# Performance work log

Measured on AMD Instinct MI355X. Metric: run time of the kernel, lower is better.

The kernel has to match this reference:

```python
import jax, jax.numpy as jnp
import numpy as np

B, S, DIM = 1, 4096, 4096
H, HL, D = 32, 8, 128          # query heads, kv heads (GQA), head_dim
BS = 8                          # sparse_block_size
SINK_TOK, WIN_TOK = 30, 30
HEAVY = 800                     # heavy_const -> Mb = HEAVY // BS top blocks
NEG = -1e30


def setup_inputs() -> dict:
    key = jax.random.key(0)
    k0, k1, k2, k3 = jax.random.split(key, 4)
    x = jax.random.normal(k0, (B, S, DIM), jnp.float32)
    freqs_cis = jax.random.uniform(k1, (S, D // 2, 2), jnp.float32)  # (cos,sin)-like pairs
    wqkv_w = jax.random.normal(k2, ((H + 2 * HL) * D, DIM), jnp.float32) * 0.02
    wo_w = jax.random.normal(k3, (DIM, DIM), jnp.float32) * 0.02
    input_pos = jnp.arange(S, dtype=jnp.int32)
    return {"x": x, "freqs_cis": freqs_cis, "wqkv_w": wqkv_w, "wo_w": wo_w, "input_pos": input_pos}


def _rope(x, fc):
    # x: [B,S,h,D], fc: [S,D/2,2]
    xr = x.reshape(*x.shape[:-1], -1, 2)            # [B,S,h,D/2,2]
    fc = fc[None, :, None]                           # [1,S,1,D/2,2]
    out = jnp.stack([xr[..., 0] * fc[..., 0] - xr[..., 1] * fc[..., 1],
                     xr[..., 1] * fc[..., 0] + xr[..., 0] * fc[..., 1]], axis=-1)
    return out.reshape(x.shape)


def reference(x, freqs_cis, wqkv_w, wo_w, input_pos):
    rep = H // HL
    Tb = (S + BS - 1) // BS
    scale = 1.0 / jnp.sqrt(jnp.float32(D))

    qkv = x @ wqkv_w.T                               # [B,S,(H+2HL)*D]
    q, k, v = jnp.split(qkv, [H * D, (H + HL) * D], axis=-1)
    q = q.reshape(B, S, H, D)
    k = k.reshape(B, S, HL, D)
    v = v.reshape(B, S, HL, D)
    q = _rope(q, freqs_cis)
    k = _rope(k, freqs_cis)

    # ---- block accumulators (KVCache.update_tokens), vectorized ----
    blk = input_pos // BS                            # [S]
    k_sum = jax.ops.segment_sum(jnp.swapaxes(k, 0, 1), blk, num_segments=Tb)  # [Tb,B,HL,D]
    cnt = jax.ops.segment_sum(jnp.ones((S,), jnp.float32), blk, num_segments=Tb)  # [Tb]
    k_rep = k_sum / jnp.maximum(cnt, 1.0)[:, None, None, None]                # block-mean keys
    k_rep_h = jnp.repeat(k_rep, rep, axis=2)        # [Tb,B,H,D] (GQA repeat)

    # ---- per-(B,H) block routing scores ----
    q_mean = q.mean(axis=1)                          # [B,H,D]
    scores = jnp.einsum('bhd,tbhd->bht', q_mean, k_rep_h) * scale  # [B,H,Tb]
    scores = jnp.where(cnt[None, None, :] > 0, scores, NEG)

    # ---- build_block_index: sink + window + topk ----
    sink_b = min((min(SINK_TOK, S) + BS - 1) // BS, Tb)
    window_b = min((min(WIN_TOK, S) + BS - 1) // BS, Tb)
    cur_block = (S - 1) // BS
    win_start = max(0, cur_block - window_b + 1)
    win_end = cur_block + 1
    sink_ids = jnp.arange(sink_b, dtype=jnp.int32)
    window_ids = jnp.arange(win_start, win_end, dtype=jnp.int32)
    Mb = max(0, min(HEAVY // BS, Tb))
    sc = scores.at[..., :sink_b].set(NEG).at[..., window_ids].set(NEG)
    top_ids = jax.lax.top_k(sc, Mb)[1].astype(jnp.int32)                      # [B,H,Mb]
    bidx = jnp.concatenate([
        jnp.broadcast_to(sink_ids, (B, H, sink_b)),
        jnp.broadcast_to(window_ids, (B, H, win_end - win_start)),
        top_ids], axis=-1)                           # [B,H,KLIST]

    # ---- gather selected block tokens ----
    tok = bidx[..., None] * BS + jnp.arange(BS, dtype=jnp.int32)              # [B,H,KLIST,BS]
    KL = bidx.shape[-1]
    tok = tok.reshape(B, H, KL * BS)                 # [B,H,Kt]
    valid = (tok >= 0) & (tok < S)
    tok_c = jnp.clip(tok, 0, S - 1)

    k_bhsd = jnp.swapaxes(jnp.repeat(k, rep, axis=2), 1, 2)  # [B,H,S,D]
    v_bhsd = jnp.swapaxes(jnp.repeat(v, rep, axis=2), 1, 2)
    Ksel = jnp.take_along_axis(k_bhsd, tok_c[..., None], axis=2)  # [B,H,Kt,D]
    Vsel = jnp.take_along_axis(v_bhsd, tok_c[..., None], axis=2)

    # ---- block-sparse attention with causal mask ----
    q_bhsd = jnp.swapaxes(q, 1, 2)                   # [B,H,S,D]
    att = jnp.einsum('bhsd,bhkd->bhsk', q_bhsd, Ksel) * scale
    mask = (tok_c[:, :, None, :] <= input_pos[None, None, :, None]) & valid[:, :, None, :]
    att = jnp.where(mask, att, NEG)
    p = jax.nn.softmax(att, axis=-1)
    out = jnp.einsum('bhsk,bhkd->bhsd', p, Vsel)     # [B,H,S,D]
    y = jnp.swapaxes(out, 1, 2).reshape(B, S, H * D) @ wo_w.T
    return y
```

## Files before the change

### kernel.cpp

```cpp
#include <hip/hip_runtime.h>
#include <hip/hip_bf16.h>

typedef unsigned short u16;
typedef unsigned int   u32;

using bf16x8 = __attribute__((ext_vector_type(8))) short;
using f32x4  = __attribute__((ext_vector_type(4))) float;

constexpr int S = 4096, DIM = 4096, H = 32, HL = 8, D = 128;
constexpr int NQKV = (H + 2 * HL) * D;
constexpr int QVW = (H + HL) * D;
constexpr int TB = S / 8;
constexpr int KL = 108;
constexpr float NEGF = -1e30f;
constexpr float SCALE = 0.08838834764831845f;

__device__ inline float bflo(u32 u) { return __builtin_bit_cast(float, u << 16); }
__device__ inline float bfhi(u32 u) { return __builtin_bit_cast(float, u & 0xFFFF0000u); }
__device__ inline u16 rne16(float f) {
  u32 b = __builtin_bit_cast(u32, f);
  return (u16)((b + 0x7FFFu + ((b >> 16) & 1u)) >> 16);
}
__device__ inline float bf2f(u16 h) { return __builtin_bit_cast(float, (u32)h << 16); }
__device__ inline u32 pk2(u16 a, u16 b) { return (u32)a | ((u32)b << 16); }

__device__ __forceinline__ void gload16(const u16* g, u16* l) {
  __builtin_amdgcn_global_load_lds(
      (__attribute__((address_space(1))) void*)g,
      (__attribute__((address_space(3))) void*)l, 16, 0, 0);
}

__device__ inline void xcd_swz(int nx, int& bx, int& by) {
  const int flat = blockIdx.y * nx + blockIdx.x;
  const int nwg = nx * gridDim.y;
  const int cpx = nwg >> 3;
  const int s = (flat & 7) * cpx + (flat >> 3);
  bx = s % nx;
  by = s / nx;
}

__global__ __launch_bounds__(256) void split_f32_kernel(
    const float* __restrict__ src, u16* __restrict__ hi, u16* __restrict__ lo) {
  const size_t i = ((size_t)blockIdx.x * 256 + threadIdx.x) * 8;
  float4 v0 = *(const float4*)(src + i);
  float4 v1 = *(const float4*)(src + i + 4);
  float f[8] = {v0.x, v0.y, v0.z, v0.w, v1.x, v1.y, v1.z, v1.w};
  u16 h[8], l[8];
#pragma unroll
  for (int j = 0; j < 8; ++j) {
    h[j] = rne16(f[j]);
    l[j] = rne16(f[j] - bf2f(h[j]));
  }
  uint4 ph, pl;
  ph.x = pk2(h[0], h[1]); ph.y = pk2(h[2], h[3]);
  ph.z = pk2(h[4], h[5]); ph.w = pk2(h[6], h[7]);
  pl.x = pk2(l[0], l[1]); pl.y = pk2(l[2], l[3]);
  pl.z = pk2(l[4], l[5]); pl.w = pk2(l[6], l[7]);
  *(uint4*)(hi + i) = ph;
  *(uint4*)(lo + i) = pl;
}

__global__ __launch_bounds__(256) void conv_wqkv_kernel(
    const float* __restrict__ src, u16* __restrict__ wqv,
    u16* __restrict__ wkh, u16* __restrict__ wkl) {
  const size_t i = ((size_t)blockIdx.x * 256 + threadIdx.x) * 8;
  float4 v0 = *(const float4*)(src + i);
  float4 v1 = *(const float4*)(src + i + 4);
  float f[8] = {v0.x, v0.y, v0.z, v0.w, v1.x, v1.y, v1.z, v1.w};
  u16 h[8];
#pragma unroll
  for (int j = 0; j < 8; ++j) h[j] = rne16(f[j]);
  uint4 ph;
  ph.x = pk2(h[0], h[1]); ph.y = pk2(h[2], h[3]);
  ph.z = pk2(h[4], h[5]); ph.w = pk2(h[6], h[7]);
  const int row = (int)(i >> 12);
  if (row < H * D) {
    *(uint4*)(wqv + i) = ph;
  } else if (row < (H + HL) * D) {
    const size_t off = i - (size_t)(H * D) * DIM;
    u16 l[8];
#pragma unroll
    for (int j = 0; j < 8; ++j) l[j] = rne16(f[j] - bf2f(h[j]));
    uint4 pl;
    pl.x = pk2(l[0], l[1]); pl.y = pk2(l[2], l[3]);
    pl.z = pk2(l[4], l[5]); pl.w = pk2(l[6], l[7]);
    *(uint4*)(wkh + off) = ph;
    *(uint4*)(wkl + off) = pl;
  } else {
    *(uint4*)(wqv + (i - (size_t)(HL * D) * DIM)) = ph;
  }
}

__global__ __launch_bounds__(256) void cast_bf16_kernel(
    const float* __restrict__ src, u16* __restrict__ dst) {
  const size_t i = ((size_t)blockIdx.x * 256 + threadIdx.x) * 8;
  float4 v0 = *(const float4*)(src + i);
  float4 v1 = *(const float4*)(src + i + 4);
  uint4 ph;
  ph.x = pk2(rne16(v0.x), rne16(v0.y));
  ph.y = pk2(rne16(v0.z), rne16(v0.w));
  ph.z = pk2(rne16(v1.x), rne16(v1.y));
  ph.w = pk2(rne16(v1.z), rne16(v1.w));
  *(uint4*)(dst + i) = ph;
}

template <bool OBF16>
__global__ __launch_bounds__(512, 2) void gemm256(
    const u16* __restrict__ A, const u16* __restrict__ B,
    void* __restrict__ Cp, int M, int N, int K, int lda, int ldb, int ldc) {
  __shared__ u16 lds[4 * 16384];
  const int tid = threadIdx.x;
  const int w = tid >> 6, lane = tid & 63;
  const int wm = w >> 2, wn = w & 3;
  const int l15 = lane & 15, g = lane >> 4;
  int bx, by;
  xcd_swz(gridDim.x, bx, by);
  const int m0 = by * 256, n0 = bx * 256;

  const u16* ga[4];
  const u16* gb[4];
#pragma unroll
  for (int r = 0; r < 4; ++r) {
    const int c = r * 512 + tid;
    const int row = c >> 3, j = c & 7;
    const int jsw = j ^ (row & 7);
    ga[r] = A + (size_t)(m0 + row) * lda + jsw * 8;
    gb[r] = B + (size_t)(n0 + row) * ldb + jsw * 8;
  }

  auto stageA = [&](int buf, int kt) {
    u16* base = lds + buf * 32768 + w * 512;
#pragma unroll
    for (int r = 0; r < 4; ++r) gload16(ga[r] + kt * 64, base + r * 4096);
  };
  auto stageB = [&](int buf, int kt) {
    u16* base = lds + buf * 32768 + 16384 + w * 512;
#pragma unroll
    for (int r = 0; r < 4; ++r) gload16(gb[r] + kt * 64, base + r * 4096);
  };

  bf16x8 afr[4][2], bfr[2][2];
  auto loadA = [&](int buf, int q) {
    const u16* Ab = lds + buf * 32768;
#pragma unroll
    for (int fr = 0; fr < 4; ++fr) {
      const int row = wm * 128 + q * 64 + fr * 16 + l15;
#pragma unroll
      for (int kh = 0; kh < 2; ++kh)
        afr[fr][kh] = *(const bf16x8*)(Ab + row * 64 + ((((kh << 2) | g)) ^ (l15 & 7)) * 8);
    }
  };
  auto loadB = [&](int buf, int r2) {
    const u16* Bb = lds + buf * 32768 + 16384;
#pragma unroll
    for (int fc = 0; fc < 2; ++fc) {
      const int row = wn * 64 + r2 * 32 + fc * 16 + l15;
#pragma unroll
      for (int kh = 0; kh < 2; ++kh)
        bfr[fc][kh] = *(const bf16x8*)(Bb + row * 64 + ((((kh << 2) | g)) ^ (l15 & 7)) * 8);
    }
  };

  f32x4 acc[8][4];
#pragma unroll
  for (int i = 0; i < 8; ++i)
#pragma unroll
    for (int j = 0; j < 4; ++j) acc[i][j] = {0.f, 0.f, 0.f, 0.f};

  auto mma = [&](int q, int r2) {
    __builtin_amdgcn_s_setprio(1);
#pragma unroll
    for (int fr = 0; fr < 4; ++fr)
#pragma unroll
      for (int fc = 0; fc < 2; ++fc)
#pragma unroll
        for (int kh = 0; kh < 2; ++kh)
          acc[q * 4 + fr][r2 * 2 + fc] = __builtin_amdgcn_mfma_f32_16x16x32_bf16(
              afr[fr][kh], bfr[fc][kh], acc[q * 4 + fr][r2 * 2 + fc], 0, 0, 0);
    __builtin_amdgcn_s_setprio(0);
  };

  stageA(0, 0);
  stageB(0, 0);
  const int NT = K / 64;
  for (int t = 0; t < NT; ++t) {
    const int cur = t & 1, nxt = cur ^ 1;
    if (t + 1 < NT) {
      stageA(nxt, t + 1);
      asm volatile("s_waitcnt vmcnt(4)" ::: "memory");
    } else {
      asm volatile("s_waitcnt vmcnt(0)" ::: "memory");
    }
    __builtin_amdgcn_sched_barrier(0);
    __builtin_amdgcn_s_barrier();
    loadA(cur, 0);
    loadB(cur, 0);
    mma(0, 0);
    __builtin_amdgcn_s_barrier();
    loadA(cur, 1);
    if (t + 1 < NT) stageB(nxt, t + 1);
    __builtin_amdgcn_s_barrier();
    mma(1, 0);
    __builtin_amdgcn_s_barrier();
    loadA(cur, 0);
    loadB(cur, 1);
    __builtin_amdgcn_s_barrier();
    mma(0, 1);
    __builtin_amdgcn_s_barrier();
    loadA(cur, 1);
    __builtin_amdgcn_s_barrier();
    mma(1, 1);
    __builtin_amdgcn_s_barrier();
  }
#pragma unroll
  for (int mf = 0; mf < 8; ++mf)
#pragma unroll
    for (int nf = 0; nf < 4; ++nf)
#pragma unroll
      for (int rg = 0; rg < 4; ++rg) {
        const int row = m0 + wm * 128 + mf * 16 + g * 4 + rg;
        const int col = n0 + wn * 64 + nf * 16 + l15;
        if constexpr (OBF16)
          ((u16*)Cp)[(size_t)row * ldc + col] = rne16(acc[mf][nf][rg]);
        else
          ((float*)Cp)[(size_t)row * ldc + col] = acc[mf][nf][rg];
      }
}

template <bool OBF16>
__global__ __launch_bounds__(256) void gemm_bf16(
    const u16* __restrict__ A, const u16* __restrict__ B,
    void* __restrict__ Cp, int M, int N, int K, int lda, int ldb, int ldc) {
  __shared__ u16 As[2][128 * 32];
  __shared__ u16 Bs[2][128 * 32];
  const int tid = threadIdx.x;
  const int lane = tid & 63;
  const int w = tid >> 6;
  const int wm = w >> 1, wn = w & 1;
  int bx, by;
  xcd_swz(gridDim.x, bx, by);
  const int m0 = by * 128, n0 = bx * 128;
  const int l15 = lane & 15, g = lane >> 4;
  const int srow = tid >> 2;
  const int scol = (tid & 3) * 8;

  const u16* ga = A + (size_t)(m0 + srow) * lda + scol;
  const u16* gb = B + (size_t)(n0 + srow) * ldb + scol;
  const size_t a64 = (size_t)64 * lda;
  const size_t b64 = (size_t)64 * ldb;

  auto stage = [&](int buf, int k0) {
    u16* lA = As[buf] + w * 512;
    u16* lB = Bs[buf] + w * 512;
    gload16(ga + k0, lA);
    gload16(ga + k0 + a64, lA + 2048);
    gload16(gb + k0, lB);
    gload16(gb + k0 + b64, lB + 2048);
  };

  f32x4 acc[4][4];
#pragma unroll
  for (int i = 0; i < 4; ++i)
#pragma unroll
    for (int j = 0; j < 4; ++j) acc[i][j] = {0.f, 0.f, 0.f, 0.f};

  stage(0, 0);
  __syncthreads();
  const int niter = K / 32;
  for (int it = 0; it < niter; ++it) {
    const int cur = it & 1;
    if (it + 1 < niter) stage(cur ^ 1, (it + 1) * 32);
    bf16x8 af[4], bfr[4];
#pragma unroll
    for (int i = 0; i < 4; ++i)
      af[i] = *(const bf16x8*)(As[cur] + (wm * 64 + i * 16 + l15) * 32 + g * 8);
#pragma unroll
    for (int j = 0; j < 4; ++j)
      bfr[j] = *(const bf16x8*)(Bs[cur] + (wn * 64 + j * 16 + l15) * 32 + g * 8);
#pragma unroll
    for (int i = 0; i < 4; ++i)
#pragma unroll
      for (int j = 0; j < 4; ++j)
        acc[i][j] = __builtin_amdgcn_mfma_f32_16x16x32_bf16(af[i], bfr[j], acc[i][j], 0, 0, 0);
    __syncthreads();
  }
#pragma unroll
  for (int i = 0; i < 4; ++i)
#pragma unroll
    for (int j = 0; j < 4; ++j)
#pragma unroll
      for (int rg = 0; rg < 4; ++rg) {
        const int row = m0 + wm * 64 + i * 16 + g * 4 + rg;
        const int col = n0 + wn * 64 + j * 16 + l15;
        if constexpr (OBF16)
          ((u16*)Cp)[(size_t)row * ldc + col] = rne16(acc[i][j][rg]);
        else
          ((float*)Cp)[(size_t)row * ldc + col] = acc[i][j][rg];
      }
}

__global__ __launch_bounds__(256) void gemm_k3(
    const u16* __restrict__ Ahg, const u16* __restrict__ Alg,
    const u16* __restrict__ Bhg, const u16* __restrict__ Blg,
    float* __restrict__ C, int M, int N, int K) {
  __shared__ u16 Ah[2][128 * 32];
  __shared__ u16 Al[2][128 * 32];
  __shared__ u16 Bh[2][64 * 32];
  __shared__ u16 Bl[2][64 * 32];
  const int tid = threadIdx.x;
  const int lane = tid & 63;
  const int w = tid >> 6;
  const int wm = w >> 1, wn = w & 1;
  int bx, by;
  xcd_swz(gridDim.x, bx, by);
  const int m0 = by * 128, n0 = bx * 64;
  const int l15 = lane & 15, g = lane >> 4;
  const int srow = tid >> 2;
  const int scol = (tid & 3) * 8;

  const u16* gah = Ahg + (size_t)(m0 + srow) * K + scol;
  const u16* gal = Alg + (size_t)(m0 + srow) * K + scol;
  const u16* gbh = Bhg + (size_t)(n0 + srow) * K + scol;
  const u16* gbl = Blg + (size_t)(n0 + srow) * K + scol;
  const size_t a64 = (size_t)64 * K;

  auto stage = [&](int buf, int k0) {
    gload16(gah + k0, Ah[buf] + w * 512);
    gload16(gah + k0 + a64, Ah[buf] + w * 512 + 2048);
    gload16(gal + k0, Al[buf] + w * 512);
    gload16(gal + k0 + a64, Al[buf] + w * 512 + 2048);
    gload16(gbh + k0, Bh[buf] + w * 512);
    gload16(gbl + k0, Bl[buf] + w * 512);
  };

  f32x4 acc[4][2];
#pragma unroll
  for (int i = 0; i < 4; ++i)
#pragma unroll
    for (int j = 0; j < 2; ++j) acc[i][j] = {0.f, 0.f, 0.f, 0.f};

  stage(0, 0);
  __syncthreads();
  const int niter = K / 32;
  for (int it = 0; it < niter; ++it) {
    const int cur = it & 1;
    if (it + 1 < niter) stage(cur ^ 1, (it + 1) * 32);
    bf16x8 fah[4], fal[4], fbh[2], fbl[2];
#pragma unroll
    for (int i = 0; i < 4; ++i) {
      fah[i] = *(const bf16x8*)(Ah[cur] + (wm * 64 + i * 16 + l15) * 32 + g * 8);
      fal[i] = *(const bf16x8*)(Al[cur] + (wm * 64 + i * 16 + l15) * 32 + g * 8);
    }
#pragma unroll
    for (int j = 0; j < 2; ++j) {
      fbh[j] = *(const bf16x8*)(Bh[cur] + (wn * 32 + j * 16 + l15) * 32 + g * 8);
      fbl[j] = *(const bf16x8*)(Bl[cur] + (wn * 32 + j * 16 + l15) * 32 + g * 8);
    }
#pragma unroll
    for (int i = 0; i < 4; ++i)
#pragma unroll
      for (int j = 0; j < 2; ++j) {
        acc[i][j] = __builtin_amdgcn_mfma_f32_16x16x32_bf16(fal[i], fbh[j], acc[i][j], 0, 0, 0);
        acc[i][j] = __builtin_amdgcn_mfma_f32_16x16x32_bf16(fah[i], fbl[j], acc[i][j], 0, 0, 0);
        acc[i][j] = __builtin_amdgcn_mfma_f32_16x16x32_bf16(fah[i], fbh[j], acc[i][j], 0, 0, 0);
      }
    __syncthreads();
  }
#pragma unroll
  for (int i = 0; i < 4; ++i)
#pragma unroll
    for (int j = 0; j < 2; ++j)
#pragma unroll
      for (int rg = 0; rg < 4; ++rg) {
        const int row = m0 + wm * 64 + i * 16 + g * 4 + rg;
        const int col = n0 + wn * 32 + j * 16 + l15;
        C[(size_t)row * N + col] = acc[i][j][rg];
      }
}

__global__ __launch_bounds__(128) void xcd_kernel(
    const float* __restrict__ x, const float* __restrict__ freqs,
    float* __restrict__ XC, float* __restrict__ XD) {
  const int d = blockIdx.x * 128 + threadIdx.x;
  const int i0 = blockIdx.y * 32;
  const int s0 = blockIdx.z * 128;
  float accC[32], accD[32];
#pragma unroll
  for (int ii = 0; ii < 32; ++ii) { accC[ii] = 0.f; accD[ii] = 0.f; }
  for (int s = s0; s < s0 + 128; ++s) {
    const float xv = x[(size_t)s * DIM + d];
    const float* fr = freqs + (size_t)s * 128 + i0 * 2;
#pragma unroll
    for (int ii = 0; ii < 32; ++ii) {
      accC[ii] += fr[2 * ii] * xv;
      accD[ii] += fr[2 * ii + 1] * xv;
    }
  }
#pragma unroll
  for (int ii = 0; ii < 32; ++ii) {
    atomicAdd(&XC[(size_t)(i0 + ii) * DIM + d], accC[ii]);
    atomicAdd(&XD[(size_t)(i0 + ii) * DIM + d], accD[ii]);
  }
}

__global__ __launch_bounds__(256) void mrow_kernel(
    const float* __restrict__ wq, const float* __restrict__ XC,
    const float* __restrict__ XD, float* __restrict__ M1, float* __restrict__ M2) {
  const int r = blockIdx.x * 4 + (threadIdx.x >> 6);
  const int lane = threadIdx.x & 63;
  const int i = (r & 127) >> 1;
  const float* wr = wq + (size_t)r * DIM;
  const float* xc = XC + (size_t)i * DIM;
  const float* xd = XD + (size_t)i * DIM;
  float s1 = 0.f, s2 = 0.f;
  for (int k = lane; k < DIM; k += 64) {
    float wv = wr[k];
    s1 += wv * xc[k];
    s2 += wv * xd[k];
  }
#pragma unroll
  for (int off = 1; off < 64; off <<= 1) {
    s1 += __shfl_xor(s1, off, 64);
    s2 += __shfl_xor(s2, off, 64);
  }
  if (lane == 0) { M1[r] = s1; M2[r] = s2; }
}

__global__ __launch_bounds__(256) void rope_q_kernel(
    const u16* __restrict__ qvb, const float* __restrict__ freqs,
    u16* __restrict__ qb) {
  const int h = blockIdx.y;
  const int s0 = blockIdx.x * 64;
  const int tid = threadIdx.x;
  const int d = tid & 127, half = tid >> 7;
  for (int pp = half; pp < 64; pp += 2) {
    const int s = s0 + pp;
    u32 pr = *(const u32*)(qvb + (size_t)s * QVW + h * D + (d & ~1));
    float a = bflo(pr), b = bfhi(pr);
    float2 fc = *(const float2*)(freqs + (size_t)s * 128 + (d & ~1));
    float o = (d & 1) ? (b * fc.x + a * fc.y) : (a * fc.x - b * fc.y);
    qb[((size_t)h * S + s) * D + d] = rne16(o);
  }
}

__global__ __launch_bounds__(128) void rope_kv_kernel(
    const float* __restrict__ kf, const u16* __restrict__ qvb,
    const float* __restrict__ freqs,
    u16* __restrict__ kb, u16* __restrict__ vbt, float* __restrict__ krep) {
  const int hl = blockIdx.y;
  const int t = blockIdx.x;
  const int d = threadIdx.x;
  float sum = 0.f;
  u16 vv[8];
#pragma unroll
  for (int pp = 0; pp < 8; ++pp) {
    const int s = t * 8 + pp;
    float2 kp = *(const float2*)(kf + (size_t)s * 1024 + hl * D + (d & ~1));
    float2 fc = *(const float2*)(freqs + (size_t)s * 128 + (d & ~1));
    float o = (d & 1) ? (kp.y * fc.x + kp.x * fc.y) : (kp.x * fc.x - kp.y * fc.y);
    kb[((size_t)hl * S + s) * D + d] = rne16(o);
    sum += o;
    vv[pp] = qvb[(size_t)s * QVW + H * D + hl * D + d];
  }
  krep[((size_t)t * HL + hl) * D + d] = sum * 0.125f;
  uint4 pk;
  pk.x = pk2(vv[0], vv[1]);
  pk.y = pk2(vv[2], vv[3]);
  pk.z = pk2(vv[4], vv[5]);
  pk.w = pk2(vv[6], vv[7]);
  *(uint4*)(vbt + ((size_t)hl * D + d) * S + t * 8) = pk;
}

__global__ __launch_bounds__(512) void topk_kernel(
    const float* __restrict__ M1, const float* __restrict__ M2,
    const float* __restrict__ krep, int* __restrict__ bidx) {
  const int h = blockIdx.x;
  const int t = threadIdx.x;
  __shared__ float qm[128];
  if (t < 128) {
    int r = h * 128 + t;
    float v = (t & 1) ? (M1[r] + M2[r - 1]) : (M1[r] - M2[r + 1]);
    qm[t] = v * (1.f / 4096.f);
  }
  __syncthreads();
  const float* kr = krep + ((size_t)t * HL + (h >> 2)) * 128;
  float s = 0.f;
#pragma unroll 8
  for (int d = 0; d < 128; ++d) s += qm[d] * kr[d];
  s *= SCALE;
  if (t < 4 || t >= 508) s = NEGF;
  if (t < 4) {
    bidx[h * KL + t] = t;
    bidx[h * KL + 4 + t] = 508 + t;
  }
  __shared__ float wv[8];
  __shared__ int wi[8];
  __shared__ int bestsh;
  for (int iter = 0; iter < 100; ++iter) {
    float v = s;
    int idx = t;
#pragma unroll
    for (int off = 1; off < 64; off <<= 1) {
      float ov = __shfl_xor(v, off, 64);
      int oi = __shfl_xor(idx, off, 64);
      if (ov > v || (ov == v && oi < idx)) { v = ov; idx = oi; }
    }
    if ((t & 63) == 0) { wv[t >> 6] = v; wi[t >> 6] = idx; }
    __syncthreads();
    if (t == 0) {
      float bv = wv[0];
      int bi = wi[0];
#pragma unroll
      for (int u = 1; u < 8; ++u)
        if (wv[u] > bv || (wv[u] == bv && wi[u] < bi)) { bv = wv[u]; bi = wi[u]; }
      bestsh = bi;
      bidx[h * KL + 8 + iter] = bi;
    }
    __syncthreads();
    if (t == bestsh) s = NEGF;
  }
}

__global__ __launch_bounds__(256) void attn_mfma(
    const u16* __restrict__ qb, const u16* __restrict__ kb,
    const u16* __restrict__ vbt, const int* __restrict__ bidx,
    u16* __restrict__ attno) {
  __shared__ u16 Ks[64][136];
  __shared__ u16 Vt[128][72];
  __shared__ u16 Ps[4][16][72];
  const int h = blockIdx.y, hl = h >> 2;
  const int q0 = blockIdx.x * 64;
  const int tid = threadIdx.x;
  const int w = tid >> 6, lane = tid & 63;
  const int l15 = lane & 15, g = lane >> 4;
  constexpr int NS = (KL + 7) / 8;

  bf16x8 qf[4];
  {
    const u16* qp = qb + ((size_t)h * S + q0 + w * 16 + l15) * D + g * 8;
#pragma unroll
    for (int c = 0; c < 4; ++c) qf[c] = *(const bf16x8*)(qp + c * 32);
  }
  f32x4 o[8];
#pragma unroll
  for (int c = 0; c < 8; ++c) o[c] = {0.f, 0.f, 0.f, 0.f};
  float mrow[4], lrow[4];
#pragma unroll
  for (int r = 0; r < 4; ++r) { mrow[r] = NEGF; lrow[r] = 0.f; }

  const int ktok = tid >> 2, kq = tid & 3;
  const int vd = tid >> 1, vh = tid & 1;

  int tb[8];
  int tbn[8];
  uint4 kreg[4], vreg[4];

  auto issue = [&](int t8) {
#pragma unroll
    for (int s = 0; s < 8; ++s) {
      const int st = t8 + s;
      tbn[s] = (st < KL) ? bidx[h * KL + st] * 8 : S + 8;
    }
    const int kslot = t8 + (ktok >> 3);
    const int kblk = (kslot < KL) ? bidx[h * KL + kslot] : 0;
    const u16* ksrc = kb + ((size_t)hl * S + kblk * 8 + (ktok & 7)) * D + kq * 32;
#pragma unroll
    for (int j = 0; j < 4; ++j) kreg[j] = *(const uint4*)(ksrc + j * 8);
    const u16* vsrc = vbt + ((size_t)hl * D + vd) * S;
#pragma unroll
    for (int j = 0; j < 4; ++j) {
      const int vslot = t8 + vh * 4 + j;
      const int vblk = (vslot < KL) ? bidx[h * KL + vslot] : 0;
      vreg[j] = *(const uint4*)(vsrc + (size_t)vblk * 8);
    }
  };
  auto store = [&]() {
#pragma unroll
    for (int j = 0; j < 4; ++j) *(uint4*)&Ks[ktok][kq * 32 + j * 8] = kreg[j];
#pragma unroll
    for (int j = 0; j < 4; ++j) *(uint4*)&Vt[vd][vh * 32 + j * 8] = vreg[j];
  };

  issue(0);
  store();
#pragma unroll
  for (int s = 0; s < 8; ++s) tb[s] = tbn[s];
  __syncthreads();

  for (int t = 0; t < NS; ++t) {
    const bool hasNext = (t + 1 < NS);
    if (hasNext) issue((t + 1) * 8);

    f32x4 sT[4];
#pragma unroll
    for (int ti = 0; ti < 4; ++ti) sT[ti] = {0.f, 0.f, 0.f, 0.f};
#pragma unroll
    for (int c = 0; c < 4; ++c)
#pragma unroll
      for (int ti = 0; ti < 4; ++ti) {
        bf16x8 kf = *(const bf16x8*)&Ks[ti * 16 + l15][c * 32 + g * 8];
        sT[ti] = __builtin_amdgcn_mfma_f32_16x16x32_bf16(qf[c], kf, sT[ti], 0, 0, 0);
      }

    int tg[4];
#pragma unroll
    for (int ti = 0; ti < 4; ++ti)
      tg[ti] = ((l15 & 8) ? tb[ti * 2 + 1] : tb[ti * 2]) + (l15 & 7);
    float p[4][4], mx[4];
#pragma unroll
    for (int r = 0; r < 4; ++r) {
      const int sq = q0 + w * 16 + g * 4 + r;
      float m = NEGF;
#pragma unroll
      for (int ti = 0; ti < 4; ++ti) {
        p[r][ti] = (tg[ti] <= sq) ? sT[ti][r] * SCALE : NEGF;
        m = fmaxf(m, p[r][ti]);
      }
      m = fmaxf(m, __shfl_xor(m, 1, 64));
      m = fmaxf(m, __shfl_xor(m, 2, 64));
      m = fmaxf(m, __shfl_xor(m, 4, 64));
      m = fmaxf(m, __shfl_xor(m, 8, 64));
      mx[r] = m;
    }
    const bool need = (mx[0] > mrow[0] + 8.f) | (mx[1] > mrow[1] + 8.f) |
                      (mx[2] > mrow[2] + 8.f) | (mx[3] > mrow[3] + 8.f);
    if (__any((int)need)) {
#pragma unroll
      for (int r = 0; r < 4; ++r) {
        const float mnew = fmaxf(mrow[r], mx[r]);
        const float alpha = __expf(mrow[r] - mnew);
        mrow[r] = mnew;
        lrow[r] *= alpha;
#pragma unroll
        for (int c = 0; c < 8; ++c) o[c][r] *= alpha;
      }
    }
#pragma unroll
    for (int r = 0; r < 4; ++r) {
      float rs = 0.f;
#pragma unroll
      for (int ti = 0; ti < 4; ++ti) {
        p[r][ti] = __expf(p[r][ti] - mrow[r]);
        rs += p[r][ti];
      }
      rs += __shfl_xor(rs, 1, 64);
      rs += __shfl_xor(rs, 2, 64);
      rs += __shfl_xor(rs, 4, 64);
      rs += __shfl_xor(rs, 8, 64);
      lrow[r] += rs;
#pragma unroll
      for (int ti = 0; ti < 4; ++ti)
        Ps[w][g * 4 + r][ti * 16 + l15] = rne16(p[r][ti]);
    }
    bf16x8 pf0 = *(const bf16x8*)&Ps[w][l15][g * 8];
    bf16x8 pf1 = *(const bf16x8*)&Ps[w][l15][32 + g * 8];
#pragma unroll
    for (int c = 0; c < 8; ++c) {
      bf16x8 v0 = *(const bf16x8*)&Vt[c * 16 + l15][g * 8];
      bf16x8 v1 = *(const bf16x8*)&Vt[c * 16 + l15][32 + g * 8];
      o[c] = __builtin_amdgcn_mfma_f32_16x16x32_bf16(pf0, v0, o[c], 0, 0, 0);
      o[c] = __builtin_amdgcn_mfma_f32_16x16x32_bf16(pf1, v1, o[c], 0, 0, 0);
    }
    __syncthreads();
    if (hasNext) {
      store();
#pragma unroll
      for (int s = 0; s < 8; ++s) tb[s] = tbn[s];
      __syncthreads();
    }
  }
  float inv[4];
#pragma unroll
  for (int r = 0; r < 4; ++r) inv[r] = 1.f / lrow[r];
#pragma unroll
  for (int c = 0; c < 8; ++c)
#pragma unroll
    for (int r = 0; r < 4; ++r)
      attno[(size_t)(q0 + w * 16 + g * 4 + r) * DIM + h * D + c * 16 + l15] =
          rne16(o[c][r] * inv[r]);
}

extern "C" void kernel_launch(void* const* d_in, const int* in_sizes, int n_in,
                              void* d_out, int out_size, void* d_ws, size_t ws_size,
                              hipStream_t stream) {
  const float* x     = (const float*)d_in[0];
  const float* freqs = (const float*)d_in[1];
  const float* wqkv  = (const float*)d_in[2];
  const float* wo    = (const float*)d_in[3];
  float* out = (float*)d_out;

  char* p = (char*)d_ws;
  auto alloc = [&](size_t bytes) {
    char* r = p;
    p += (bytes + 255) & ~(size_t)255;
    return r;
  };
  u16*   xh   = (u16*)alloc((size_t)S * DIM * 2);
  u16*   xl   = (u16*)alloc((size_t)S * DIM * 2);
  u16*   wqv  = (u16*)alloc((size_t)QVW * DIM * 2);
  u16*   wkh  = (u16*)alloc((size_t)HL * D * DIM * 2);
  u16*   wkl  = (u16*)alloc((size_t)HL * D * DIM * 2);
  u16*   wob  = (u16*)alloc((size_t)DIM * DIM * 2);
  u16*   qvb  = (u16*)alloc((size_t)S * QVW * 2);
  float* kf32 = (float*)alloc((size_t)S * HL * D * 4);
  u16*   qb   = (u16*)alloc((size_t)H * S * D * 2);
  u16*   kb   = (u16*)alloc((size_t)HL * S * D * 2);
  u16*   vbt  = (u16*)alloc((size_t)HL * D * S * 2);
  float* krep = (float*)alloc((size_t)TB * HL * D * 4);
  float* XC   = (float*)alloc((size_t)64 * DIM * 4);
  float* XD   = (float*)alloc((size_t)64 * DIM * 4);
  float* M1   = (float*)alloc((size_t)H * D * 4);
  float* M2   = (float*)alloc((size_t)H * D * 4);
  int*   bidx = (int*)alloc((size_t)H * KL * 4);
  u16*   attno = (u16*)alloc((size_t)S * DIM * 2);

  hipMemsetAsync(XC, 0, (size_t)64 * DIM * 4, stream);
  hipMemsetAsync(XD, 0, (size_t)64 * DIM * 4, stream);

  split_f32_kernel<<<(S * DIM) / 2048, 256, 0, stream>>>(x, xh, xl);
  conv_wqkv_kernel<<<(NQKV * DIM) / 2048, 256, 0, stream>>>(wqkv, wqv, wkh, wkl);
  cast_bf16_kernel<<<(DIM * DIM) / 2048, 256, 0, stream>>>(wo, wob);

  gemm256<true><<<dim3((H * D) / 256, S / 256), 512, 0, stream>>>(
      xh, wqv, qvb, S, H * D, DIM, DIM, DIM, QVW);
  gemm_bf16<true><<<dim3((HL * D) / 128, S / 128), 256, 0, stream>>>(
      xh, wqv + (size_t)(H * D) * DIM, qvb + H * D, S, HL * D, DIM, DIM, DIM, QVW);

  gemm_k3<<<dim3((HL * D) / 64, S / 128), 256, 0, stream>>>(
      xh, xl, wkh, wkl, kf32, S, HL * D, DIM);

  xcd_kernel<<<dim3(32, 2, 32), 128, 0, stream>>>(x, freqs, XC, XD);
  mrow_kernel<<<1024, 256, 0, stream>>>(wqkv, XC, XD, M1, M2);
  rope_q_kernel<<<dim3(S / 64, H), 256, 0, stream>>>(qvb, freqs, qb);
  rope_kv_kernel<<<dim3(TB, HL), 128, 0, stream>>>(kf32, qvb, freqs, kb, vbt, krep);
  topk_kernel<<<H, 512, 0, stream>>>(M1, M2, krep, bidx);
  attn_mfma<<<dim3(S / 64, H), 256, 0, stream>>>(qb, kb, vbt, bidx, attno);
  gemm256<false><<<dim3(DIM / 256, S / 256), 512, 0, stream>>>(
      attno, wob, out, S, DIM, DIM, DIM, DIM, DIM);
}
```

Baseline: 1.461 ms.

## Double-buffer K/V tiles in attention with XOR-swizzled LDS and single barrier

The sparse attention kernel now keeps two LDS buffers for K and V tiles. The next tile is stored into the alternate buffer right after the QK MFMAs, which removes the second __syncthreads per iteration. LDS padding is replaced by XOR swizzling on 16-byte chunks for the K, V and P tiles to avoid bank conflicts while shrinking the row stride. Block indices are reloaded each iteration instead of being carried in registers, and launch bounds request two blocks per CU, which may raise register pressure.

```diff
diff --git a/kernel.cpp b/kernel.cpp
--- a/kernel.cpp
+++ b/kernel.cpp
@@ -521,18 +521,19 @@
   }
 }
 
-__global__ __launch_bounds__(256) void attn_mfma(
+__global__ __launch_bounds__(256, 2) void attn_mfma(
     const u16* __restrict__ qb, const u16* __restrict__ kb,
     const u16* __restrict__ vbt, const int* __restrict__ bidx,
     u16* __restrict__ attno) {
-  __shared__ u16 Ks[64][136];
-  __shared__ u16 Vt[128][72];
-  __shared__ u16 Ps[4][16][72];
+  __shared__ u16 Ks[2][64][128];
+  __shared__ u16 Vt[2][128][64];
+  __shared__ u16 Ps[4][16][64];
   const int h = blockIdx.y, hl = h >> 2;
   const int q0 = blockIdx.x * 64;
   const int tid = threadIdx.x;
   const int w = tid >> 6, lane = tid & 63;
   const int l15 = lane & 15, g = lane >> 4;
+  const int l7 = l15 & 7;
   constexpr int NS = (KL + 7) / 8;
 
   bf16x8 qf[4];
@@ -549,18 +550,13 @@
   for (int r = 0; r < 4; ++r) { mrow[r] = NEGF; lrow[r] = 0.f; }
 
   const int ktok = tid >> 2, kq = tid & 3;
+  const int kx = ktok & 7;
   const int vd = tid >> 1, vh = tid & 1;
-
-  int tb[8];
-  int tbn[8];
+  const int vx = vd & 7;
+
   uint4 kreg[4], vreg[4];
 
   auto issue = [&](int t8) {
-#pragma unroll
-    for (int s = 0; s < 8; ++s) {
-      const int st = t8 + s;
-      tbn[s] = (st < KL) ? bidx[h * KL + st] * 8 : S + 8;
-    }
     const int kslot = t8 + (ktok >> 3);
     const int kblk = (kslot < KL) ? bidx[h * KL + kslot] : 0;
     const u16* ksrc = kb + ((size_t)hl * S + kblk * 8 + (ktok & 7)) * D + kq * 32;
@@ -574,21 +570,28 @@
       vreg[j] = *(const uint4*)(vsrc + (size_t)vblk * 8);
     }
   };
-  auto store = [&]() {
-#pragma unroll
-    for (int j = 0; j < 4; ++j) *(uint4*)&Ks[ktok][kq * 32 + j * 8] = kreg[j];
-#pragma unroll
-    for (int j = 0; j < 4; ++j) *(uint4*)&Vt[vd][vh * 32 + j * 8] = vreg[j];
+  auto store = [&](int buf) {
+#pragma unroll
+    for (int j = 0; j < 4; ++j)
+      *(uint4*)&Ks[buf][ktok][((kq * 4 + j) ^ kx) * 8] = kreg[j];
+#pragma unroll
+    for (int j = 0; j < 4; ++j)
+      *(uint4*)&Vt[buf][vd][((vh * 4 + j) ^ vx) * 8] = vreg[j];
   };
 
   issue(0);
-  store();
-#pragma unroll
-  for (int s = 0; s < 8; ++s) tb[s] = tbn[s];
+  store(0);
   __syncthreads();
 
   for (int t = 0; t < NS; ++t) {
+    const int cur = t & 1;
     const bool hasNext = (t + 1 < NS);
+    int tb[8];
+#pragma unroll
+    for (int s = 0; s < 8; ++s) {
+      const int st = t * 8 + s;
+      tb[s] = (st < KL) ? bidx[h * KL + st] * 8 : S + 8;
+    }
     if (hasNext) issue((t + 1) * 8);
 
     f32x4 sT[4];
@@ -598,9 +601,11 @@
     for (int c = 0; c < 4; ++c)
 #pragma unroll
       for (int ti = 0; ti < 4; ++ti) {
-        bf16x8 kf = *(const bf16x8*)&Ks[ti * 16 + l15][c * 32 + g * 8];
+        bf16x8 kf = *(const bf16x8*)&Ks[cur][ti * 16 + l15][((c * 4 + g) ^ l7) * 8];
         sT[ti] = __builtin_amdgcn_mfma_f32_16x16x32_bf16(qf[c], kf, sT[ti], 0, 0, 0);
       }
+
+    if (hasNext) store(cur ^ 1);
 
     int tg[4];
 #pragma unroll
@@ -648,26 +653,25 @@
       rs += __shfl_xor(rs, 4, 64);
       rs += __shfl_xor(rs, 8, 64);
       lrow[r] += rs;
-#pragma unroll
-      for (int ti = 0; ti < 4; ++ti)
-        Ps[w][g * 4 + r][ti * 16 + l15] = rne16(p[r][ti]);
-    }
-    bf16x8 pf0 = *(const bf16x8*)&Ps[w][l15][g * 8];
-    bf16x8 pf1 = *(const bf16x8*)&Ps[w][l15][32 + g * 8];
+      const int prow = g * 4 + r;
+      const int px = prow & 7;
+#pragma unroll
+      for (int ti = 0; ti < 4; ++ti) {
+        const int ch = ti * 2 + (l15 >> 3);
+        Ps[w][prow][((ch ^ px) * 8) + l7] = rne16(p[r][ti]);
+      }
+    }
+    bf16x8 pf0 = *(const bf16x8*)&Ps[w][l15][(g ^ l7) * 8];
+    bf16x8 pf1 = *(const bf16x8*)&Ps[w][l15][((4 + g) ^ l7) * 8];
 #pragma unroll
     for (int c = 0; c < 8; ++c) {
-      bf16x8 v0 = *(const bf16x8*)&Vt[c * 16 + l15][g * 8];
-      bf16x8 v1 = *(const bf16x8*)&Vt[c * 16 + l15][32 + g * 8];
+      const int vrow = c * 16 + l15;
+      bf16x8 v0 = *(const bf16x8*)&Vt[cur][vrow][(g ^ l7) * 8];
+      bf16x8 v1 = *(const bf16x8*)&Vt[cur][vrow][((4 + g) ^ l7) * 8];
       o[c] = __builtin_amdgcn_mfma_f32_16x16x32_bf16(pf0, v0, o[c], 0, 0, 0);
       o[c] = __builtin_amdgcn_mfma_f32_16x16x32_bf16(pf1, v1, o[c], 0, 0, 0);
     }
     __syncthreads();
-    if (hasNext) {
-      store();
-#pragma unroll
-      for (int s = 0; s < 8; ++s) tb[s] = tbn[s];
-      __syncthreads();
-    }
   }
   float inv[4];
 #pragma unroll
```

After: 1.403 ms. 1.04x faster.
